# Kernel tuning notes

Measured on AMD Instinct MI355X. Metric: run time of the kernel, lower is better.

Reference implementation:

```python
import jax, jax.numpy as jnp
import numpy as np

NUM_HEADS = 16  # concat repeats the identical head output this many times


def setup_inputs() -> dict:
    key = jax.random.key(0)
    ks = jax.random.split(key, 6)
    B, S, E, D = 4, 4096, 1024, 64  # D = E // NUM_HEADS
    s_in = 1.0 / np.sqrt(E)
    return {
        "x": jax.random.normal(ks[0], (B, S, E), dtype=jnp.float32),
        "Wq": jax.random.normal(ks[1], (E, D), dtype=jnp.float32) * s_in,
        "bq": jnp.zeros((D,), dtype=jnp.float32),
        "Wk": jax.random.normal(ks[2], (E, D), dtype=jnp.float32) * s_in,
        "bk": jnp.zeros((D,), dtype=jnp.float32),
        "Wv": jax.random.normal(ks[3], (E, D), dtype=jnp.float32) * s_in,
        "bv": jnp.zeros((D,), dtype=jnp.float32),
        "Wo": jax.random.normal(ks[4], (E, E), dtype=jnp.float32) * s_in,
        "bo": jnp.zeros((E,), dtype=jnp.float32),
    }


def reference(x, Wq, bq, Wk, bk, Wv, bv, Wo, bo):
    # Single shared projection to head_dim (the torch code projects E -> E//H once).
    q = x @ Wq + bq          # [B,S,D]
    k = x @ Wk + bk          # [B,S,D]
    v = x @ Wv + bv          # [B,S,D]
    d = q.shape[-1]
    scale = 1.0 / jnp.sqrt(jnp.asarray(d, dtype=q.dtype))
    scores = jnp.einsum("bqd,bkd->bqk", q, k) * scale   # [B,S,S]
    attn = jax.nn.softmax(scores, axis=-1)
    ctx = jnp.einsum("bqk,bkd->bqd", attn, v)            # [B,S,D]
    # Every head computes the identical result; concat == tile along features.
    cat = jnp.tile(ctx, (1, 1, NUM_HEADS))               # [B,S,E]
    return cat @ Wo + bo
```

## Files before the change

kernel.cpp:

```cpp
#include <hip/hip_runtime.h>
#include <hip/hip_bf16.h>

#define BB 4
#define SS 4096
#define EE 1024
#define DD 64

typedef unsigned short u16;
typedef unsigned int   u32;
typedef __bf16 bf16_t;
typedef bf16_t bf16x2 __attribute__((ext_vector_type(2)));
typedef bf16_t bf16x8 __attribute__((ext_vector_type(8)));
typedef float  f32x4  __attribute__((ext_vector_type(4)));
typedef u32    u32x4  __attribute__((ext_vector_type(4)));

__device__ __forceinline__ u16 f2bf_hw(float f) {
    bf16_t b = (bf16_t)f;
    u16 u; __builtin_memcpy(&u, &b, 2);
    return u;
}
__device__ __forceinline__ void bfsplit(float v, u16& h, u16& l) {
    bf16_t hb = (bf16_t)v;
    float hf = (float)hb;
    __builtin_memcpy(&h, &hb, 2);
    bf16_t lb = (bf16_t)(v - hf);
    __builtin_memcpy(&l, &lb, 2);
}

__global__ __launch_bounds__(256) void prep_kernel(const float* __restrict__ Wq,
                                                   const float* __restrict__ Wk,
                                                   const float* __restrict__ Wv,
                                                   const float* __restrict__ Wo,
                                                   u16* __restrict__ Wt,
                                                   u16* __restrict__ WoTh,
                                                   u16* __restrict__ WoTl) {
    const int b = blockIdx.x;
    const int tid = threadIdx.x;
    if (b < 768) {
        int t = b * 256 + tid;
        int c = t >> 10, e = t & 1023;
        const float* W = (c < 64) ? Wq : (c < 128) ? Wk : Wv;
        Wt[c * 1024 + e] = f2bf_hw(W[e * 64 + (c & 63)]);
        return;
    }
    const int t = (b - 768) * 256 + tid;
    const int d = t >> 10, e = t & 1023;
    float s = 0.f;
    #pragma unroll
    for (int h = 0; h < 16; h++) s += Wo[(h * 64 + d) * 1024 + e];
    u16 hh, ll;
    bfsplit(s, hh, ll);
    WoTh[e * 64 + d] = hh;
    WoTl[e * 64 + d] = ll;
}

__global__ __launch_bounds__(256) void proj_kernel(const float* __restrict__ x,
                                                   const u16* __restrict__ Wtg,
                                                   const float* __restrict__ bq,
                                                   const float* __restrict__ bk,
                                                   const float* __restrict__ bv,
                                                   u16* __restrict__ Qg,
                                                   u16* __restrict__ Kg,
                                                   u16* __restrict__ Vtg) {
    __shared__ __align__(16) u16 xt[32 * 136];
    __shared__ __align__(16) u16 wts[192 * 136];

    const int tid  = threadIdx.x;
    const int w    = tid >> 6;
    const int lane = tid & 63;
    const int m    = lane & 15;
    const int quad = lane >> 4;
    const int r0   = blockIdx.x * 32;
    const int mt   = w & 1;
    const int ch   = w >> 1;

    f32x4 acc[6];
    #pragma unroll
    for (int i = 0; i < 6; i++) acc[i] = (f32x4){0.f, 0.f, 0.f, 0.f};

    f32x4 xr[4];
    u32x4 wr[12];

    auto preload = [&](int kb) {
        #pragma unroll
        for (int j = 0; j < 2; j++) {
            const int id = tid + j * 256, row = id >> 4, seg = id & 15;
            const float* src = x + (r0 + row) * 1024 + kb * 128 + seg * 8;
            xr[2 * j]     = *(const f32x4*)(src);
            xr[2 * j + 1] = *(const f32x4*)(src + 4);
        }
        #pragma unroll
        for (int j = 0; j < 12; j++) {
            const int id = tid + j * 256, row = id >> 4, seg = id & 15;
            wr[j] = *(const u32x4*)(Wtg + row * 1024 + kb * 128 + seg * 8);
        }
    };
    auto commit = [&]() {
        #pragma unroll
        for (int j = 0; j < 2; j++) {
            const int id = tid + j * 256, row = id >> 4, seg = id & 15;
            bf16x8 v;
            #pragma unroll
            for (int k = 0; k < 4; k++) {
                v[k]     = (bf16_t)xr[2 * j][k];
                v[4 + k] = (bf16_t)xr[2 * j + 1][k];
            }
            *(bf16x8*)(xt + row * 136 + seg * 8) = v;
        }
        #pragma unroll
        for (int j = 0; j < 12; j++) {
            const int id = tid + j * 256, row = id >> 4, seg = id & 15;
            *(u32x4*)(wts + row * 136 + seg * 8) = wr[j];
        }
    };

    preload(0);
    for (int kb = 0; kb < 8; kb++) {
        __syncthreads();
        commit();
        __syncthreads();
        if (kb < 7) preload(kb + 1);
        #pragma unroll
        for (int ks = 0; ks < 4; ks++) {
            bf16x8 a = *(const bf16x8*)(xt + (mt * 16 + m) * 136 + ks * 32 + quad * 8);
            #pragma unroll
            for (int c = 0; c < 6; c++) {
                bf16x8 b = *(const bf16x8*)(wts + (ch * 96 + c * 16 + m) * 136 + ks * 32 + quad * 8);
                acc[c] = __builtin_amdgcn_mfma_f32_16x16x32_bf16(a, b, acc[c], 0, 0, 0);
            }
        }
    }

    const int rbase = r0 + mt * 16 + quad * 4;
    #pragma unroll
    for (int c = 0; c < 6; c++) {
        const int col   = ch * 96 + c * 16 + m;
        const int which = col >> 6;
        const int d     = col & 63;
        const float bias = (which == 0 ? bq : which == 1 ? bk : bv)[d];
        #pragma unroll
        for (int r = 0; r < 4; r++) {
            const int row = rbase + r;
            float v = acc[c][r] + bias;
            if (which == 0) {
                Qg[row * 64 + d] = f2bf_hw(v * 0.125f);
            } else if (which == 1) {
                Kg[row * 64 + d] = f2bf_hw(v);
            } else {
                const int b = row >> 12, s = row & 4095;
                const int sp = (s & ~31) | ((s & 12) << 1) | (s & 3) | ((s >> 2) & 4);
                Vtg[(b * 64 + d) * 4096 + sp] = f2bf_hw(v);
            }
        }
    }
}

#define ATTN_LDS 73728
__global__ __launch_bounds__(512) void attn_kernel(const u16* __restrict__ Qg,
                                                   const u16* __restrict__ Kg,
                                                   const u16* __restrict__ Vtg,
                                                   float* __restrict__ ctxP,
                                                   float* __restrict__ liP) {
    extern __shared__ __align__(16) u16 smem[];

    const int tid  = threadIdx.x;
    const int w    = tid >> 6;
    const int lane = tid & 63;
    const int m    = lane & 15;
    const int quad = lane >> 4;
    const int kg   = w >> 1;
    const int qg   = w & 1;

    const int bi    = blockIdx.x;
    const int khalf = bi & 1;
    const int batch = (bi >> 1) & 3;
    const int qt    = bi >> 3;
    const int qrow0 = batch * 4096 + qt * 64;

    u16* Kt = smem + w * 4608;
    u16* Vt = Kt + 2048;

    bf16x8 aq[2][2];
    #pragma unroll
    for (int s = 0; s < 2; s++) {
        const int qr = qrow0 + qg * 32 + s * 16 + m;
        aq[s][0] = *(const bf16x8*)(Qg + qr * 64 + quad * 8);
        aq[s][1] = *(const bf16x8*)(Qg + qr * 64 + 32 + quad * 8);
    }

    f32x4 acc[2][4];
    float li[2] = {0.f, 0.f};
    #pragma unroll
    for (int s = 0; s < 2; s++)
        #pragma unroll
        for (int c = 0; c < 4; c++) acc[s][c] = (f32x4){0.f, 0.f, 0.f, 0.f};

    const u16* Kbase = Kg + (batch * 4096 + khalf * 2048) * 64;
    const u16* Vbase = Vtg + batch * 64 * 4096 + khalf * 2048;

    const int kr8  = lane >> 3, kseg = lane & 7;
    const int vr4  = lane >> 2, vseg = lane & 3;

    u32x4 kr[4], vr[4];
    auto preload = [&](int it) {
        const int k0 = it * 128 + kg * 32;
        #pragma unroll
        for (int i = 0; i < 4; i++) {
            kr[i] = *(const u32x4*)(Kbase + (k0 + kr8 + 8 * i) * 64 + kseg * 8);
            vr[i] = *(const u32x4*)(Vbase + (vr4 + 16 * i) * 4096 + k0 + vseg * 8);
        }
    };
    auto commit = [&]() {
        #pragma unroll
        for (int i = 0; i < 4; i++) {
            *(u32x4*)(Kt + (kr8 + 8 * i) * 64 + ((kseg ^ kr8) * 8)) = kr[i];
            *(u32x4*)(Vt + (vr4 + 16 * i) * 40 + vseg * 8) = vr[i];
        }
    };

    const float LOG2E = 1.4426950408889634f;
    const float NC2   = -12.0f * 1.4426950408889634f;

    preload(0);
    commit();

    for (int it = 0; it < 16; it++) {
        if (it < 15) preload(it + 1);

        f32x4 sc[2][2];
        __builtin_amdgcn_s_setprio(1);
        #pragma unroll
        for (int c = 0; c < 2; c++) {
            const int row = c * 16 + m;
            bf16x8 k0f = *(const bf16x8*)(Kt + row * 64 + ((quad ^ (m & 7)) * 8));
            bf16x8 k1f = *(const bf16x8*)(Kt + row * 64 + (((quad | 4) ^ (m & 7)) * 8));
            #pragma unroll
            for (int s = 0; s < 2; s++) {
                f32x4 t = __builtin_amdgcn_mfma_f32_16x16x32_bf16(k0f, aq[s][0], (f32x4){0.f,0.f,0.f,0.f}, 0, 0, 0);
                sc[s][c] = __builtin_amdgcn_mfma_f32_16x16x32_bf16(k1f, aq[s][1], t, 0, 0, 0);
            }
        }
        __builtin_amdgcn_s_setprio(0);

        bf16x8 pa[2];
        #pragma unroll
        for (int s = 0; s < 2; s++) {
            float p[8];
            #pragma unroll
            for (int r = 0; r < 4; r++) {
                p[r]     = __builtin_exp2f(__builtin_fmaf(sc[s][0][r], LOG2E, NC2));
                p[4 + r] = __builtin_exp2f(__builtin_fmaf(sc[s][1][r], LOG2E, NC2));
            }
            li[s] += ((p[0] + p[1]) + (p[2] + p[3])) + ((p[4] + p[5]) + (p[6] + p[7]));
            #pragma unroll
            for (int j = 0; j < 8; j++) pa[s][j] = (bf16_t)p[j];
        }

        __builtin_amdgcn_s_setprio(1);
        #pragma unroll
        for (int c = 0; c < 4; c++) {
            bf16x8 bv = *(const bf16x8*)(Vt + (c * 16 + m) * 40 + quad * 8);
            #pragma unroll
            for (int s = 0; s < 2; s++)
                acc[s][c] = __builtin_amdgcn_mfma_f32_16x16x32_bf16(pa[s], bv, acc[s][c], 0, 0, 0);
        }
        __builtin_amdgcn_s_setprio(0);

        if (it < 15) {
            asm volatile("s_waitcnt lgkmcnt(0)" ::: "memory");
            commit();
        }
    }

    #pragma unroll
    for (int s = 0; s < 2; s++) {
        float v = li[s];
        v += __shfl_xor(v, 16);
        v += __shfl_xor(v, 32);
        li[s] = v;
    }

    __syncthreads();
    float* mf = (float*)smem;
    float* cb = mf + w * 2208;
    #pragma unroll
    for (int s = 0; s < 2; s++)
        #pragma unroll
        for (int c = 0; c < 4; c++)
            #pragma unroll
            for (int r = 0; r < 4; r++)
                cb[(s * 16 + quad * 4 + r) * 68 + c * 16 + m] = acc[s][c][r];
    if (lane < 16) {
        #pragma unroll
        for (int s = 0; s < 2; s++) cb[2176 + s * 16 + m] = li[s];
    }
    __syncthreads();

    const int q  = tid >> 3;
    const int d0 = (tid & 7) * 8;
    const int qgq = q >> 5;
    const int ql  = q & 31;
    float L = 0.f;
    f32x4 o0 = (f32x4){0.f, 0.f, 0.f, 0.f};
    f32x4 o1 = (f32x4){0.f, 0.f, 0.f, 0.f};
    #pragma unroll
    for (int g = 0; g < 4; g++) {
        const float* c2 = mf + (g * 2 + qgq) * 2208;
        L  += c2[2176 + ql];
        o0 += *(const f32x4*)(c2 + ql * 68 + d0);
        o1 += *(const f32x4*)(c2 + ql * 68 + d0 + 4);
    }
    const int gr = khalf * 16384 + qrow0 + q;
    *(f32x4*)(ctxP + gr * 64 + d0)     = o0;
    *(f32x4*)(ctxP + gr * 64 + d0 + 4) = o1;
    if ((tid & 7) == 0) liP[gr] = L;
}

__global__ __launch_bounds__(256) void out_kernel(const float* __restrict__ ctxP,
                                                  const float* __restrict__ liP,
                                                  const u16* __restrict__ WoTh,
                                                  const u16* __restrict__ WoTl,
                                                  const float* __restrict__ bo,
                                                  float* __restrict__ out) {
    __shared__ __align__(16) u16 ldsH[64 * 72];
    __shared__ __align__(16) u16 ldsL[64 * 72];
    const int tid = threadIdx.x;
    const int r0  = (blockIdx.x >> 2) * 64;
    const int eb  = (blockIdx.x & 3) * 256;

    {
        const int q  = tid >> 2;
        const int dq = (tid & 3) * 16;
        const float inv = 1.0f / (liP[r0 + q] + liP[16384 + r0 + q]);
        const float* A = ctxP + (r0 + q) * 64 + dq;
        const float* B = ctxP + 16384 * 64 + (r0 + q) * 64 + dq;
        #pragma unroll
        for (int i = 0; i < 4; i++) {
            f32x4 a4 = *(const f32x4*)(A + i * 4);
            f32x4 b4 = *(const f32x4*)(B + i * 4);
            f32x4 o  = (a4 + b4) * inv;
            u16 h[4], l[4];
            #pragma unroll
            for (int k = 0; k < 4; k++) bfsplit(o[k], h[k], l[k]);
            u32 h0 = (u32)h[0] | ((u32)h[1] << 16);
            u32 h1 = (u32)h[2] | ((u32)h[3] << 16);
            u32 l0 = (u32)l[0] | ((u32)l[1] << 16);
            u32 l1 = (u32)l[2] | ((u32)l[3] << 16);
            const int off = q * 72 + dq + i * 4;
            *(u32*)(ldsH + off)     = h0;
            *(u32*)(ldsH + off + 2) = h1;
            *(u32*)(ldsL + off)     = l0;
            *(u32*)(ldsL + off + 2) = l1;
        }
    }
    __syncthreads();

    const int w    = tid >> 6;
    const int lane = tid & 63;
    const int m    = lane & 15;
    const int quad = lane >> 4;
    const int wr   = w >> 1;
    const int wc   = w & 1;

    bf16x8 aH[2][2], aL[2][2];
    #pragma unroll
    for (int rs = 0; rs < 2; rs++)
        #pragma unroll
        for (int ks = 0; ks < 2; ks++) {
            const int off = (wr * 32 + rs * 16 + m) * 72 + ks * 32 + quad * 8;
            aH[rs][ks] = *(const bf16x8*)(ldsH + off);
            aL[rs][ks] = *(const bf16x8*)(ldsL + off);
        }

    f32x4 acc[2][8];
    #pragma unroll
    for (int rs = 0; rs < 2; rs++)
        #pragma unroll
        for (int cs = 0; cs < 8; cs++) acc[rs][cs] = (f32x4){0.f, 0.f, 0.f, 0.f};

    #pragma unroll
    for (int cs = 0; cs < 8; cs++) {
        const int e = eb + wc * 128 + cs * 16 + m;
        bf16x8 bh0 = *(const bf16x8*)(WoTh + e * 64 + quad * 8);
        bf16x8 bh1 = *(const bf16x8*)(WoTh + e * 64 + 32 + quad * 8);
        bf16x8 bl0 = *(const bf16x8*)(WoTl + e * 64 + quad * 8);
        bf16x8 bl1 = *(const bf16x8*)(WoTl + e * 64 + 32 + quad * 8);
        #pragma unroll
        for (int rs = 0; rs < 2; rs++) {
            f32x4 t = acc[rs][cs];
            t = __builtin_amdgcn_mfma_f32_16x16x32_bf16(aH[rs][0], bh0, t, 0, 0, 0);
            t = __builtin_amdgcn_mfma_f32_16x16x32_bf16(aH[rs][1], bh1, t, 0, 0, 0);
            t = __builtin_amdgcn_mfma_f32_16x16x32_bf16(aL[rs][0], bh0, t, 0, 0, 0);
            t = __builtin_amdgcn_mfma_f32_16x16x32_bf16(aL[rs][1], bh1, t, 0, 0, 0);
            t = __builtin_amdgcn_mfma_f32_16x16x32_bf16(aH[rs][0], bl0, t, 0, 0, 0);
            t = __builtin_amdgcn_mfma_f32_16x16x32_bf16(aH[rs][1], bl1, t, 0, 0, 0);
            acc[rs][cs] = t;
        }
    }

    #pragma unroll
    for (int cs = 0; cs < 8; cs++) {
        const int e = eb + wc * 128 + cs * 16 + m;
        const float bov = bo[e];
        #pragma unroll
        for (int rs = 0; rs < 2; rs++) {
            const int row = r0 + wr * 32 + rs * 16 + quad * 4;
            #pragma unroll
            for (int r = 0; r < 4; r++)
                out[(row + r) * 1024 + e] = acc[rs][cs][r] + bov;
        }
    }
}

extern "C" void kernel_launch(void* const* d_in, const int* in_sizes, int n_in,
                              void* d_out, int out_size, void* d_ws, size_t ws_size,
                              hipStream_t stream) {
    const float* x  = (const float*)d_in[0];
    const float* Wq = (const float*)d_in[1];
    const float* bq = (const float*)d_in[2];
    const float* Wk = (const float*)d_in[3];
    const float* bk = (const float*)d_in[4];
    const float* Wv = (const float*)d_in[5];
    const float* bv = (const float*)d_in[6];
    const float* Wo = (const float*)d_in[7];
    const float* bo = (const float*)d_in[8];
    float* out = (float*)d_out;

    char* ws = (char*)d_ws;
    u16*   Wt   = (u16*)(ws);
    u16*   WoTh = (u16*)(ws + 393216);
    u16*   WoTl = (u16*)(ws + 524288);
    u16*   Qg   = (u16*)(ws + 655360);
    u16*   Kg   = (u16*)(ws + 2752512);
    u16*   Vtg  = (u16*)(ws + 4849664);
    float* ctxP = (float*)(ws + 6946816);
    float* liP  = (float*)(ws + 15335424);

    (void)hipFuncSetAttribute((const void*)attn_kernel,
                              hipFuncAttributeMaxDynamicSharedMemorySize, ATTN_LDS);

    prep_kernel <<<1024, 256, 0, stream>>>(Wq, Wk, Wv, Wo, Wt, WoTh, WoTl);
    proj_kernel <<<512,  256, 0, stream>>>(x, Wt, bq, bk, bv, Qg, Kg, Vtg);
    attn_kernel <<<512,  512, ATTN_LDS, stream>>>(Qg, Kg, Vtg, ctxP, liP);
    out_kernel  <<<1024, 256, 0, stream>>>(ctxP, liP, WoTh, WoTl, bo, out);
}
```

Baseline: 201.6 us.

## Load K and V MFMA fragments directly from global memory, bypassing LDS staging

The attention loop no longer stages K and V tiles through per-wave shared memory. Each lane now loads its MFMA operand fragments straight from global memory into registers, with K for the next step prefetched after the score MFMAs and V loaded at the start of each step. This removes the LDS writes and reads, the lgkmcnt wait, and a barrier, and shrinks the LDS allocation. The cost is less latency hiding for V, since it is loaded in the same iteration that uses it, and direct-to-fragment global reads that are less coalesced and rely on the cache.

New measurement: 230.0 us. 1.14x slower.

```diff
diff --git a/kernel.cpp b/kernel.cpp
--- a/kernel.cpp
+++ b/kernel.cpp
@@ -155,7 +155,7 @@
     }
 }
 
-#define ATTN_LDS 73728
+#define ATTN_LDS 70656
 __global__ __launch_bounds__(512) void attn_kernel(const u16* __restrict__ Qg,
                                                    const u16* __restrict__ Kg,
                                                    const u16* __restrict__ Vtg,
@@ -177,9 +177,6 @@
     const int qt    = bi >> 3;
     const int qrow0 = batch * 4096 + qt * 64;
 
-    u16* Kt = smem + w * 4608;
-    u16* Vt = Kt + 2048;
-
     bf16x8 aq[2][2];
     #pragma unroll
     for (int s = 0; s < 2; s++) {
@@ -195,52 +192,46 @@
         #pragma unroll
         for (int c = 0; c < 4; c++) acc[s][c] = (f32x4){0.f, 0.f, 0.f, 0.f};
 
-    const u16* Kbase = Kg + (batch * 4096 + khalf * 2048) * 64;
-    const u16* Vbase = Vtg + batch * 64 * 4096 + khalf * 2048;
-
-    const int kr8  = lane >> 3, kseg = lane & 7;
-    const int vr4  = lane >> 2, vseg = lane & 3;
-
-    u32x4 kr[4], vr[4];
-    auto preload = [&](int it) {
+    const u16* Kb = Kg + (batch * 4096 + khalf * 2048) * 64;
+    const u16* Vb = Vtg + batch * 64 * 4096 + khalf * 2048;
+
+    bf16x8 kf[2][2], vf[4];
+    auto loadK = [&](int it) {
         const int k0 = it * 128 + kg * 32;
         #pragma unroll
-        for (int i = 0; i < 4; i++) {
-            kr[i] = *(const u32x4*)(Kbase + (k0 + kr8 + 8 * i) * 64 + kseg * 8);
-            vr[i] = *(const u32x4*)(Vbase + (vr4 + 16 * i) * 4096 + k0 + vseg * 8);
+        for (int c = 0; c < 2; c++) {
+            const u16* p = Kb + (k0 + c * 16 + m) * 64 + quad * 8;
+            kf[c][0] = *(const bf16x8*)(p);
+            kf[c][1] = *(const bf16x8*)(p + 32);
         }
     };
-    auto commit = [&]() {
-        #pragma unroll
-        for (int i = 0; i < 4; i++) {
-            *(u32x4*)(Kt + (kr8 + 8 * i) * 64 + ((kseg ^ kr8) * 8)) = kr[i];
-            *(u32x4*)(Vt + (vr4 + 16 * i) * 40 + vseg * 8) = vr[i];
-        }
+    auto loadV = [&](int it) {
+        const int k0 = it * 128 + kg * 32;
+        #pragma unroll
+        for (int c = 0; c < 4; c++)
+            vf[c] = *(const bf16x8*)(Vb + (c * 16 + m) * 4096 + k0 + quad * 8);
     };
 
     const float LOG2E = 1.4426950408889634f;
     const float NC2   = -12.0f * 1.4426950408889634f;
 
-    preload(0);
-    commit();
-
+    loadK(0);
     for (int it = 0; it < 16; it++) {
-        if (it < 15) preload(it + 1);
+        loadV(it);
 
         f32x4 sc[2][2];
         __builtin_amdgcn_s_setprio(1);
         #pragma unroll
         for (int c = 0; c < 2; c++) {
-            const int row = c * 16 + m;
-            bf16x8 k0f = *(const bf16x8*)(Kt + row * 64 + ((quad ^ (m & 7)) * 8));
-            bf16x8 k1f = *(const bf16x8*)(Kt + row * 64 + (((quad | 4) ^ (m & 7)) * 8));
             #pragma unroll
             for (int s = 0; s < 2; s++) {
-                f32x4 t = __builtin_amdgcn_mfma_f32_16x16x32_bf16(k0f, aq[s][0], (f32x4){0.f,0.f,0.f,0.f}, 0, 0, 0);
-                sc[s][c] = __builtin_amdgcn_mfma_f32_16x16x32_bf16(k1f, aq[s][1], t, 0, 0, 0);
+                f32x4 t = __builtin_amdgcn_mfma_f32_16x16x32_bf16(kf[c][0], aq[s][0], (f32x4){0.f,0.f,0.f,0.f}, 0, 0, 0);
+                sc[s][c] = __builtin_amdgcn_mfma_f32_16x16x32_bf16(kf[c][1], aq[s][1], t, 0, 0, 0);
             }
         }
         __builtin_amdgcn_s_setprio(0);
+
+        if (it < 15) loadK(it + 1);
 
         bf16x8 pa[2];
         #pragma unroll
@@ -259,17 +250,11 @@
         __builtin_amdgcn_s_setprio(1);
         #pragma unroll
         for (int c = 0; c < 4; c++) {
-            bf16x8 bv = *(const bf16x8*)(Vt + (c * 16 + m) * 40 + quad * 8);
             #pragma unroll
             for (int s = 0; s < 2; s++)
-                acc[s][c] = __builtin_amdgcn_mfma_f32_16x16x32_bf16(pa[s], bv, acc[s][c], 0, 0, 0);
+                acc[s][c] = __builtin_amdgcn_mfma_f32_16x16x32_bf16(pa[s], vf[c], acc[s][c], 0, 0, 0);
         }
         __builtin_amdgcn_s_setprio(0);
-
-        if (it < 15) {
-            asm volatile("s_waitcnt lgkmcnt(0)" ::: "memory");
-            commit();
-        }
     }
 
     #pragma unroll
@@ -280,7 +265,6 @@
         li[s] = v;
     }
 
-    __syncthreads();
     float* mf = (float*)smem;
     float* cb = mf + w * 2208;
     #pragma unroll
```
